# Optimization experiments

Hardware: AMD Instinct MI355X
Metric: run time of the kernel (lower is better)

The kernel has to match this reference:

```python
import jax, jax.numpy as jnp
import numpy as np

D_MODEL = 1024
HEADS = 16
DK = D_MODEL // HEADS  # 64
B, S = 1, 4096


def setup_inputs() -> dict:
    key = jax.random.key(0)
    ks = jax.random.split(key, 11)
    sd = 1.0 / np.sqrt(D_MODEL)
    return {
        "q": jax.random.normal(ks[0], (B, S, D_MODEL), jnp.float32),
        "k": jax.random.normal(ks[1], (B, S, D_MODEL), jnp.float32),
        "v": jax.random.normal(ks[2], (B, S, D_MODEL), jnp.float32),
        "Wq": jax.random.uniform(ks[3], (D_MODEL, D_MODEL), jnp.float32, -sd, sd),
        "bq": jax.random.uniform(ks[4], (D_MODEL,), jnp.float32, -sd, sd),
        "Wk": jax.random.uniform(ks[5], (D_MODEL, DK), jnp.float32, -sd, sd),
        "bk": jax.random.uniform(ks[6], (DK,), jnp.float32, -sd, sd),
        "Wv": jax.random.uniform(ks[7], (D_MODEL, DK), jnp.float32, -sd, sd),
        "bv": jax.random.uniform(ks[8], (DK,), jnp.float32, -sd, sd),
        "Wo": jax.random.uniform(ks[9], (D_MODEL, D_MODEL), jnp.float32, -sd, sd),
        "bo": jax.random.uniform(ks[10], (D_MODEL,), jnp.float32, -sd, sd),
    }


def reference(q, k, v, Wq, bq, Wk, bk, Wv, bv, Wo, bo):
    b, s, d = q.shape
    # projections: q -> [b, H, s, dk]; k, v -> single shared head [b, s, dk]
    qp = (q @ Wq + bq).reshape(b, s, HEADS, DK).transpose(0, 2, 1, 3)
    kp = k @ Wk + bk  # [b, s, dk]
    vp = v @ Wv + bv  # [b, s, dk]
    # NOTE: original module never applies self.scale or dropout — faithful.
    scores = jnp.einsum('bhqd,bkd->bhqk', qp, kp)  # [b, H, s, s]
    attn = jax.nn.softmax(scores, axis=-1)
    out = jnp.einsum('bhqk,bkd->bhqd', attn, vp)  # [b, H, s, dk]
    out = out.transpose(0, 2, 1, 3).reshape(b, s, d)
    return out @ Wo + bo
```

## Files before the change

### kernel.cpp

```cpp
#include <hip/hip_runtime.h>
#include <hip/hip_bf16.h>
#include <stdint.h>

typedef __bf16 bf16_t;
typedef __attribute__((ext_vector_type(8))) __bf16 bf16x8;
typedef __attribute__((ext_vector_type(4))) __bf16 bf16x4;
typedef __attribute__((ext_vector_type(4))) float f32x4;

#define S_LEN 4096
#define DMODEL 1024
#define NHEADS 16
#define DKH 64

#if defined(__has_builtin)
#if __has_builtin(__builtin_amdgcn_exp2f)
#define EXP2F(x) __builtin_amdgcn_exp2f(x)
#endif
#endif
#ifndef EXP2F
#define EXP2F(x) __expf((x)*0.6931471805599453f)
#endif

__device__ __forceinline__ f32x4 mfma16(bf16x8 a, bf16x8 b, f32x4 c) {
  return __builtin_amdgcn_mfma_f32_16x16x32_bf16(a, b, c, 0, 0, 0);
}

template <typename TS>
__device__ __forceinline__ bf16x8 load8_bf16(const TS* g) {
  bf16x8 o;
  if constexpr (sizeof(TS) == 4) {
    const float4 f0 = *(const float4*)(g);
    const float4 f1 = *(const float4*)(g + 4);
    o[0] = (bf16_t)f0.x; o[1] = (bf16_t)f0.y; o[2] = (bf16_t)f0.z; o[3] = (bf16_t)f0.w;
    o[4] = (bf16_t)f1.x; o[5] = (bf16_t)f1.y; o[6] = (bf16_t)f1.z; o[7] = (bf16_t)f1.w;
  } else {
    o = *(const bf16x8*)(g);
  }
  return o;
}

template <typename TS>
__device__ __forceinline__ void stage_tile64(const TS* __restrict__ g, int gstride,
                                             bf16_t* lds, int rows, int tid) {
  for (int i = tid; i < rows * 8; i += 256) {
    const int row = i >> 3, j = i & 7;
    const int c = j ^ (row & 7);
    bf16x8 v = load8_bf16(g + (size_t)row * gstride + j * 8);
    *(bf16x8*)((char*)lds + row * 128 + c * 16) = v;
  }
}

__device__ __forceinline__ bf16x8 frag64(const bf16_t* lds, int row, int g) {
  return *(const bf16x8*)((const char*)lds + row * 128 + ((g ^ (row & 7)) * 16));
}

__device__ __forceinline__ void gload16(const bf16_t* g, bf16_t* lds) {
  __builtin_amdgcn_global_load_lds(
      (const __attribute__((address_space(1))) unsigned int*)g,
      (__attribute__((address_space(3))) unsigned int*)lds, 16, 0, 0);
}

__global__ __launch_bounds__(256) void convert_bf16(const float* __restrict__ src,
                                                    bf16_t* __restrict__ dst) {
  const size_t i = (size_t)(blockIdx.x * 256 + threadIdx.x) * 8;
  bf16x8 v = load8_bf16(src + i);
  *(bf16x8*)(dst + i) = v;
}

__global__ __launch_bounds__(256) void prep_weights(const float* __restrict__ Wq,
                                                    const float* __restrict__ Wo,
                                                    const float* __restrict__ Wk,
                                                    const float* __restrict__ Wv,
                                                    const float* __restrict__ qsrc,
                                                    bf16_t* __restrict__ Wqt,
                                                    bf16_t* __restrict__ Wot,
                                                    bf16_t* __restrict__ Wkt,
                                                    bf16_t* __restrict__ Wvt,
                                                    bf16_t* __restrict__ qdst) {
  const int b = blockIdx.x;
  const int tid = threadIdx.x;
  if (b >= 544) {
    const size_t i = ((size_t)(b - 544) * 256 + tid) * 8;
    bf16x8 v = load8_bf16(qsrc + i);
    *(bf16x8*)(qdst + i) = v;
    return;
  }
  const float* src; bf16_t* dst; int ss, ds_, bx, by;
  if (b < 256)      { src = Wq; dst = Wqt; ss = 1024; ds_ = 1024; bx = b & 15;         by = b >> 4; }
  else if (b < 512) { src = Wo; dst = Wot; ss = 1024; ds_ = 1024; bx = (b - 256) & 15; by = (b - 256) >> 4; }
  else if (b < 528) { src = Wk; dst = Wkt; ss = 64;   ds_ = 1024; bx = 0;              by = b - 512; }
  else              { src = Wv; dst = Wvt; ss = 64;   ds_ = 1024; bx = 0;              by = b - 528; }

  __shared__ bf16_t t[64][65];
  const int r0 = by * 64, c0 = bx * 64;
#pragma unroll
  for (int it = 0; it < 2; ++it) {
    int idx = tid + it * 256;
    int r = idx >> 3, c8 = idx & 7;
    bf16x8 v = load8_bf16(src + (size_t)(r0 + r) * ss + c0 + c8 * 8);
#pragma unroll
    for (int j = 0; j < 8; ++j) t[c8 * 8 + j][r] = v[j];
  }
  __syncthreads();
#pragma unroll
  for (int it = 0; it < 2; ++it) {
    int idx = tid + it * 256;
    int r = idx >> 3, c8 = idx & 7;
    bf16x8 v;
#pragma unroll
    for (int j = 0; j < 8; ++j) v[j] = t[r][c8 * 8 + j];
    *(bf16x8*)(dst + (size_t)(c0 + r) * ds_ + r0 + c8 * 8) = v;
  }
}

template <typename TC>
__global__ __launch_bounds__(256) void gemm_nt_dma(const bf16_t* __restrict__ A, int lda,
                                                   const bf16_t* __restrict__ Bt, int ldb,
                                                   const float* __restrict__ bias,
                                                   TC* __restrict__ C, int ldc, int K,
                                                   float escale) {
  constexpr int BM = 128, BN = 64;
  __shared__ __align__(16) bf16_t As[2][BM * 64];
  __shared__ __align__(16) bf16_t Bs[2][BN * 64];
  const int tid = threadIdx.x, l = tid & 63, w = tid >> 6;
  const int lr = l & 15, quad = l >> 4;
  const int m0 = blockIdx.y * BM, n0 = blockIdx.x * BN;
  const int wm = w * 32;

  const int srow = l >> 3;
  const int sch = (l & 7) ^ srow;
  const bf16_t* a0 = A + (size_t)(m0 + w * 32 + srow) * lda + sch * 8;
  const bf16_t* b0 = Bt + (size_t)(n0 + w * 16 + srow) * ldb + sch * 8;

  f32x4 zero = {0.f, 0.f, 0.f, 0.f};
  f32x4 acc[2][4];
#pragma unroll
  for (int i = 0; i < 2; ++i)
#pragma unroll
    for (int j = 0; j < 4; ++j) acc[i][j] = zero;

  const int nt = K >> 6;

#pragma unroll
  for (int sub = 0; sub < 4; ++sub)
    gload16(a0 + (size_t)sub * 8 * lda, &As[0][(w * 32 + sub * 8) * 64]);
#pragma unroll
  for (int sub = 0; sub < 2; ++sub)
    gload16(b0 + (size_t)sub * 8 * ldb, &Bs[0][(w * 16 + sub * 8) * 64]);
  asm volatile("s_waitcnt vmcnt(0)" ::: "memory");
  __builtin_amdgcn_s_barrier();
  asm volatile("" ::: "memory");

  for (int t = 0; t < nt; ++t) {
    const int cur = t & 1;
    if (t + 1 < nt) {
#pragma unroll
      for (int sub = 0; sub < 4; ++sub)
        gload16(a0 + (size_t)(t + 1) * 64 + (size_t)sub * 8 * lda,
                &As[cur ^ 1][(w * 32 + sub * 8) * 64]);
#pragma unroll
      for (int sub = 0; sub < 2; ++sub)
        gload16(b0 + (size_t)(t + 1) * 64 + (size_t)sub * 8 * ldb,
                &Bs[cur ^ 1][(w * 16 + sub * 8) * 64]);
    }
    const bf16_t* Ac = &As[cur][0];
    const bf16_t* Bc = &Bs[cur][0];
#pragma unroll
    for (int kc = 0; kc < 2; ++kc) {
      bf16x8 af[2], bfr[4];
#pragma unroll
      for (int rt = 0; rt < 2; ++rt) af[rt] = frag64(Ac, wm + rt * 16 + lr, kc * 4 + quad);
#pragma unroll
      for (int ct = 0; ct < 4; ++ct) bfr[ct] = frag64(Bc, ct * 16 + lr, kc * 4 + quad);
#pragma unroll
      for (int rt = 0; rt < 2; ++rt)
#pragma unroll
        for (int ct = 0; ct < 4; ++ct) acc[rt][ct] = mfma16(af[rt], bfr[ct], acc[rt][ct]);
    }
    asm volatile("s_waitcnt vmcnt(0) lgkmcnt(0)" ::: "memory");
    __builtin_amdgcn_s_barrier();
    asm volatile("" ::: "memory");
  }

#pragma unroll
  for (int rt = 0; rt < 2; ++rt)
#pragma unroll
    for (int ct = 0; ct < 4; ++ct) {
      const int n = n0 + ct * 16 + lr;
      const float bv = bias[n];
      const int mb = m0 + wm + rt * 16 + quad * 4;
#pragma unroll
      for (int r = 0; r < 4; ++r)
        C[(size_t)(mb + r) * ldc + n] = (TC)((acc[rt][ct][r] + bv) * escale);
    }
}

template <int KSPLIT>
__global__ __launch_bounds__(256) void gemm_projkv_partial(const float* __restrict__ Ak,
                                                           const float* __restrict__ Av,
                                                           const bf16_t* __restrict__ Wkt,
                                                           const bf16_t* __restrict__ Wvt,
                                                           float* __restrict__ Pk,
                                                           float* __restrict__ Pv) {
  const float* A = blockIdx.z ? Av : Ak;
  const bf16_t* Bt = blockIdx.z ? Wvt : Wkt;
  float* part = blockIdx.z ? Pv : Pk;

  __shared__ __align__(16) bf16_t As[128 * 64];
  __shared__ __align__(16) bf16_t Bs[64 * 64];
  const int tid = threadIdx.x, l = tid & 63, w = tid >> 6;
  const int lr = l & 15, quad = l >> 4;
  const int kp = blockIdx.x, m0 = blockIdx.y * 128;
  const int kBase = kp * (DMODEL / KSPLIT);
  const int wm = w * 32;

  f32x4 zero = {0.f, 0.f, 0.f, 0.f};
  f32x4 acc[2][4];
#pragma unroll
  for (int i = 0; i < 2; ++i)
#pragma unroll
    for (int j = 0; j < 4; ++j) acc[i][j] = zero;

  for (int t = 0; t < (DMODEL / KSPLIT) / 64; ++t) {
    __syncthreads();
    stage_tile64(A + (size_t)m0 * DMODEL + kBase + t * 64, DMODEL, As, 128, tid);
    stage_tile64(Bt + kBase + t * 64, DMODEL, Bs, 64, tid);
    __syncthreads();
#pragma unroll
    for (int kc = 0; kc < 2; ++kc) {
      bf16x8 af[2], bfr[4];
#pragma unroll
      for (int rt = 0; rt < 2; ++rt) af[rt] = frag64(As, wm + rt * 16 + lr, kc * 4 + quad);
#pragma unroll
      for (int ct = 0; ct < 4; ++ct) bfr[ct] = frag64(Bs, ct * 16 + lr, kc * 4 + quad);
#pragma unroll
      for (int rt = 0; rt < 2; ++rt)
#pragma unroll
        for (int ct = 0; ct < 4; ++ct) acc[rt][ct] = mfma16(af[rt], bfr[ct], acc[rt][ct]);
    }
  }
#pragma unroll
  for (int rt = 0; rt < 2; ++rt)
#pragma unroll
    for (int ct = 0; ct < 4; ++ct) {
      const int n = ct * 16 + lr;
      const int mb = m0 + wm + rt * 16 + quad * 4;
#pragma unroll
      for (int r = 0; r < 4; ++r)
        part[(size_t)kp * S_LEN * 64 + (size_t)(mb + r) * 64 + n] = acc[rt][ct][r];
    }
}

__global__ __launch_bounds__(512) void reduce_kv(const float* __restrict__ Pk,
                                                 const float* __restrict__ Pv,
                                                 const float* __restrict__ bk,
                                                 const float* __restrict__ bv,
                                                 bf16_t* __restrict__ kvb,
                                                 bf16_t* __restrict__ vtb) {
  __shared__ bf16_t t[32][65];
  const int tid = threadIdx.x;
  const int s0 = blockIdx.x * 32;
  const int d = tid & 63;
  const int sgrp = tid >> 6;
  const float bkd = bk[d], bvd = bv[d];
#pragma unroll
  for (int i = 0; i < 4; ++i) {
    const int s_local = sgrp * 4 + i;
    const int gid = (s0 + s_local) * 64 + d;
    float sk = bkd, sv = bvd;
#pragma unroll
    for (int p = 0; p < 8; ++p) {
      sk += Pk[(size_t)p * S_LEN * 64 + gid];
      sv += Pv[(size_t)p * S_LEN * 64 + gid];
    }
    kvb[(size_t)(s0 + s_local) * 128 + d] = (bf16_t)sk;
    kvb[(size_t)(s0 + s_local) * 128 + 64 + d] = (bf16_t)sv;
    t[s_local][d] = (bf16_t)sv;
  }
  __syncthreads();
  if (tid < 256) {
    const int dl = tid >> 2;
    const int s8 = tid & 3;
    bf16x8 v;
#pragma unroll
    for (int j = 0; j < 8; ++j) v[j] = t[s8 * 8 + j][dl];
    *(bf16x8*)(vtb + (size_t)dl * S_LEN + s0 + s8 * 8) = v;
  }
}

__global__ __launch_bounds__(512, 4) void mqa_attn(const bf16_t* __restrict__ qp,
                                                   const bf16_t* __restrict__ kvb,
                                                   const bf16_t* __restrict__ vtb,
                                                   bf16_t* __restrict__ outp) {
  __shared__ __align__(16) char smem[49152];
  bf16_t* Ks = (bf16_t*)smem;
  bf16_t* Vs = (bf16_t*)(smem + 16384);
  char*   Ps = smem + 32768;

  const int tid = threadIdx.x, l = tid & 63, w = tid >> 6;
  const int lr = l & 15, quad = l >> 4;
  const int wq = w >> 1, wk = w & 1;
  const int h = blockIdx.y;
  const int q0 = blockIdx.x * 128;
  const int qrA = q0 + wq * 32 + lr;
  const int qrB = qrA + 16;
  char* Pw = Ps + w * 2048;

  const int srow = w * 8 + (l >> 3);
  const int schunk = (l & 7) ^ (srow & 7);
  const bf16_t* ksrc = kvb + (size_t)srow * 128 + schunk * 8;
  const bf16_t* vsrc = vtb + (size_t)srow * S_LEN + schunk * 8;

  const bf16_t* qbA = qp + (size_t)qrA * DMODEL + h * DKH;
  const bf16x8 qfA0 = *(const bf16x8*)(qbA + quad * 8);
  const bf16x8 qfA1 = *(const bf16x8*)(qbA + 32 + quad * 8);
  const bf16_t* qbB = qp + (size_t)qrB * DMODEL + h * DKH;
  const bf16x8 qfB0 = *(const bf16x8*)(qbB + quad * 8);
  const bf16x8 qfB1 = *(const bf16x8*)(qbB + 32 + quad * 8);

  f32x4 zero = {0.f, 0.f, 0.f, 0.f};
  f32x4 o[4][2];
#pragma unroll
  for (int dt = 0; dt < 4; ++dt) { o[dt][0] = zero; o[dt][1] = zero; }
  float liA = 0.f, liB = 0.f;

  gload16(ksrc, Ks + w * 512);
  gload16(vsrc, Vs + w * 512);
  asm volatile("s_waitcnt vmcnt(0)" ::: "memory");
  __builtin_amdgcn_s_barrier();
  asm volatile("" ::: "memory");

  for (int t = 0; t < S_LEN / 64; ++t) {
    const int cur = t & 1;
    if (t + 1 < S_LEN / 64) {
      gload16(ksrc + (size_t)(t + 1) * 8192, Ks + (cur ^ 1) * 4096 + w * 512);
      gload16(vsrc + (size_t)(t + 1) * 64, Vs + (cur ^ 1) * 4096 + w * 512);
    }
    const bf16_t* Kc = Ks + cur * 4096;
    const bf16_t* Vc = Vs + cur * 4096;

    f32x4 st[2][2];
#pragma unroll
    for (int kt = 0; kt < 2; ++kt) {
      const int krow = wk * 32 + kt * 16 + lr;
      const bf16x8 kf0 = frag64(Kc, krow, quad);
      const bf16x8 kf1 = frag64(Kc, krow, 4 + quad);
      f32x4 a0 = mfma16(kf0, qfA0, zero);
      a0 = mfma16(kf1, qfA1, a0);
      st[kt][0] = a0;
      f32x4 a1 = mfma16(kf0, qfB0, zero);
      a1 = mfma16(kf1, qfB1, a1);
      st[kt][1] = a1;
    }

#pragma unroll
    for (int kt = 0; kt < 2; ++kt)
#pragma unroll
      for (int qt = 0; qt < 2; ++qt) {
        bf16x4 pk;
        float rs = 0.f;
#pragma unroll
        for (int r = 0; r < 4; ++r) {
          const float p = EXP2F(st[kt][qt][r]);
          rs += p;
          pk[r] = (bf16_t)p;
        }
        if (qt == 0) liA += rs; else liB += rs;
        *(bf16x4*)(Pw + lr * 128 +
                   ((((qt << 2) + (kt << 1) + (quad >> 1)) ^ (lr & 7)) << 4) +
                   ((quad & 1) << 3)) = pk;
      }
    asm volatile("s_waitcnt lgkmcnt(0)" ::: "memory");

    const bf16x8 pf0 = *(const bf16x8*)(Pw + lr * 128 + ((quad ^ (lr & 7)) << 4));
    const bf16x8 pf1 = *(const bf16x8*)(Pw + lr * 128 + (((4 + quad) ^ (lr & 7)) << 4));
#pragma unroll
    for (int dt = 0; dt < 4; ++dt) {
      const bf16x8 vf = frag64(Vc, dt * 16 + lr, wk * 4 + quad);
      o[dt][0] = mfma16(vf, pf0, o[dt][0]);
      o[dt][1] = mfma16(vf, pf1, o[dt][1]);
    }

    asm volatile("s_waitcnt vmcnt(0) lgkmcnt(0)" ::: "memory");
    __builtin_amdgcn_s_barrier();
    asm volatile("" ::: "memory");
  }

  liA += __shfl_xor(liA, 16, 64);
  liA += __shfl_xor(liA, 32, 64);
  liB += __shfl_xor(liB, 16, 64);
  liB += __shfl_xor(liB, 32, 64);

  float* liBuf = (float*)Ps;
  if (quad == 0) {
    liBuf[w * 32 + lr] = liA;
    liBuf[w * 32 + 16 + lr] = liB;
  }
  float* Obuf = (float*)smem;
  if (wk == 1) {
#pragma unroll
    for (int dt = 0; dt < 4; ++dt)
#pragma unroll
      for (int qt = 0; qt < 2; ++qt)
        *(f32x4*)(&Obuf[wq * 2048 + (qt * 16 + lr) * 64 + dt * 16 + quad * 4]) = o[dt][qt];
  }
  __syncthreads();
  if (wk == 0) {
    const float ltA = liA + liBuf[(w ^ 1) * 32 + lr];
    const float ltB = liB + liBuf[(w ^ 1) * 32 + 16 + lr];
    const float invA = 1.f / ltA;
    const float invB = 1.f / ltB;
#pragma unroll
    for (int dt = 0; dt < 4; ++dt) {
      const f32x4 pA = *(const f32x4*)(&Obuf[wq * 2048 + lr * 64 + dt * 16 + quad * 4]);
      const f32x4 pB = *(const f32x4*)(&Obuf[wq * 2048 + (16 + lr) * 64 + dt * 16 + quad * 4]);
      bf16x4 ovA, ovB;
#pragma unroll
      for (int rg = 0; rg < 4; ++rg) {
        ovA[rg] = (bf16_t)((o[dt][0][rg] + pA[rg]) * invA);
        ovB[rg] = (bf16_t)((o[dt][1][rg] + pB[rg]) * invB);
      }
      *(bf16x4*)(outp + (size_t)qrA * DMODEL + h * DKH + dt * 16 + quad * 4) = ovA;
      *(bf16x4*)(outp + (size_t)qrB * DMODEL + h * DKH + dt * 16 + quad * 4) = ovB;
    }
  }
}

extern "C" void kernel_launch(void* const* d_in, const int* in_sizes, int n_in,
                              void* d_out, int out_size, void* d_ws, size_t ws_size,
                              hipStream_t stream) {
  const float* q  = (const float*)d_in[0];
  const float* k  = (const float*)d_in[1];
  const float* v  = (const float*)d_in[2];
  const float* Wq = (const float*)d_in[3];
  const float* bq = (const float*)d_in[4];
  const float* Wk = (const float*)d_in[5];
  const float* bk = (const float*)d_in[6];
  const float* Wv = (const float*)d_in[7];
  const float* bv = (const float*)d_in[8];
  const float* Wo = (const float*)d_in[9];
  const float* bo = (const float*)d_in[10];
  float* out = (float*)d_out;
  char* ws = (char*)d_ws;

  const size_t MB = 1u << 20;
  bf16_t* Wqt = (bf16_t*)(ws);
  bf16_t* Wot = (bf16_t*)(ws + 2 * MB);
  bf16_t* Wkt = (bf16_t*)(ws + 4 * MB);
  bf16_t* Wvt = (bf16_t*)(ws + 4 * MB + 131072);
  bf16_t* kvb = (bf16_t*)(ws + 4 * MB + 524288);
  bf16_t* vtb = (bf16_t*)(ws + 5 * MB + 524288);
  float*  Pk   = (float*)(ws + 6 * MB);
  float*  Pv   = (float*)(ws + 14 * MB);
  bf16_t* qp   = (bf16_t*)(ws + 14 * MB);
  bf16_t* attn = (bf16_t*)(ws + 6 * MB);

  const bool bigws = ws_size >= (size_t)30 * MB;
  bf16_t* qb = bigws ? (bf16_t*)(ws + 22 * MB) : (bf16_t*)(ws + 6 * MB);

  dim3 B(256);
  prep_weights<<<dim3(bigws ? 2592 : 544), B, 0, stream>>>(Wq, Wo, Wk, Wv, q,
                                                           Wqt, Wot, Wkt, Wvt, qb);

  gemm_projkv_partial<8><<<dim3(8, 32, 2), B, 0, stream>>>(k, v, Wkt, Wvt, Pk, Pv);
  reduce_kv<<<dim3(128), dim3(512), 0, stream>>>(Pk, Pv, bk, bv, kvb, vtb);

  if (!bigws) convert_bf16<<<dim3(2048), B, 0, stream>>>(q, qb);
  gemm_nt_dma<bf16_t><<<dim3(16, 32), B, 0, stream>>>(qb, 1024, Wqt, 1024, bq, qp, 1024, 1024,
                                                      1.44269504088896340736f);

  mqa_attn<<<dim3(32, 16), dim3(512), 0, stream>>>(qp, kvb, vtb, attn);

  gemm_nt_dma<float><<<dim3(16, 32), B, 0, stream>>>(attn, 1024, Wot, 1024, bo, out, 1024, 1024,
                                                     1.0f);
}
```

Baseline: 236.3 us.

## Merge Q projection and split-K KV projection into one launch

On the large-workspace path, the Q projection GEMM and the K/V partial projection GEMMs now run inside a single kernel (mid_gemms), with the block index choosing which body to run. The K/V split-K factor drops from 8 to 4 so both fit in one grid of 768 blocks. The aim is to remove a kernel launch and its tail, and to let the small K/V work fill the GPU alongside the Q GEMM. In exchange, each K/V block does more serial K work, and the shared 48KB LDS footprint may lower occupancy for the projkv blocks.

Measured after the change: 230.3 us, median of 2. 1.03x faster.

```diff
diff --git a/kernel.cpp b/kernel.cpp
--- a/kernel.cpp
+++ b/kernel.cpp
@@ -114,23 +114,110 @@
 }
 
 template <typename TC>
+__device__ __forceinline__ void gemm_body_dma(char* smem,
+                                              const bf16_t* __restrict__ A, int lda,
+                                              const bf16_t* __restrict__ Bt, int ldb,
+                                              const float* __restrict__ bias,
+                                              TC* __restrict__ C, int ldc, int K,
+                                              float escale, int m0, int n0) {
+  constexpr int BM = 128, BN = 64;
+  bf16_t* As = (bf16_t*)smem;
+  bf16_t* Bs = (bf16_t*)(smem + 32768);
+  const int tid = threadIdx.x, l = tid & 63, w = tid >> 6;
+  const int lr = l & 15, quad = l >> 4;
+  const int wm = w * 32;
+
+  const int srow = l >> 3;
+  const int sch = (l & 7) ^ srow;
+  const bf16_t* a0 = A + (size_t)(m0 + w * 32 + srow) * lda + sch * 8;
+  const bf16_t* b0 = Bt + (size_t)(n0 + w * 16 + srow) * ldb + sch * 8;
+
+  f32x4 zero = {0.f, 0.f, 0.f, 0.f};
+  f32x4 acc[2][4];
+#pragma unroll
+  for (int i = 0; i < 2; ++i)
+#pragma unroll
+    for (int j = 0; j < 4; ++j) acc[i][j] = zero;
+
+  const int nt = K >> 6;
+
+#pragma unroll
+  for (int sub = 0; sub < 4; ++sub)
+    gload16(a0 + (size_t)sub * 8 * lda, &As[(w * 32 + sub * 8) * 64]);
+#pragma unroll
+  for (int sub = 0; sub < 2; ++sub)
+    gload16(b0 + (size_t)sub * 8 * ldb, &Bs[(w * 16 + sub * 8) * 64]);
+  asm volatile("s_waitcnt vmcnt(0)" ::: "memory");
+  __builtin_amdgcn_s_barrier();
+  asm volatile("" ::: "memory");
+
+  for (int t = 0; t < nt; ++t) {
+    const int cur = t & 1;
+    if (t + 1 < nt) {
+#pragma unroll
+      for (int sub = 0; sub < 4; ++sub)
+        gload16(a0 + (size_t)(t + 1) * 64 + (size_t)sub * 8 * lda,
+                &As[(cur ^ 1) * BM * 64 + (w * 32 + sub * 8) * 64]);
+#pragma unroll
+      for (int sub = 0; sub < 2; ++sub)
+        gload16(b0 + (size_t)(t + 1) * 64 + (size_t)sub * 8 * ldb,
+                &Bs[(cur ^ 1) * BN * 64 + (w * 16 + sub * 8) * 64]);
+    }
+    const bf16_t* Ac = &As[cur * BM * 64];
+    const bf16_t* Bc = &Bs[cur * BN * 64];
+#pragma unroll
+    for (int kc = 0; kc < 2; ++kc) {
+      bf16x8 af[2], bfr[4];
+#pragma unroll
+      for (int rt = 0; rt < 2; ++rt) af[rt] = frag64(Ac, wm + rt * 16 + lr, kc * 4 + quad);
+#pragma unroll
+      for (int ct = 0; ct < 4; ++ct) bfr[ct] = frag64(Bc, ct * 16 + lr, kc * 4 + quad);
+#pragma unroll
+      for (int rt = 0; rt < 2; ++rt)
+#pragma unroll
+        for (int ct = 0; ct < 4; ++ct) acc[rt][ct] = mfma16(af[rt], bfr[ct], acc[rt][ct]);
+    }
+    asm volatile("s_waitcnt vmcnt(0) lgkmcnt(0)" ::: "memory");
+    __builtin_amdgcn_s_barrier();
+    asm volatile("" ::: "memory");
+  }
+
+#pragma unroll
+  for (int rt = 0; rt < 2; ++rt)
+#pragma unroll
+    for (int ct = 0; ct < 4; ++ct) {
+      const int n = n0 + ct * 16 + lr;
+      const float bv = bias[n];
+      const int mb = m0 + wm + rt * 16 + quad * 4;
+#pragma unroll
+      for (int r = 0; r < 4; ++r)
+        C[(size_t)(mb + r) * ldc + n] = (TC)((acc[rt][ct][r] + bv) * escale);
+    }
+}
+
+template <typename TC>
 __global__ __launch_bounds__(256) void gemm_nt_dma(const bf16_t* __restrict__ A, int lda,
                                                    const bf16_t* __restrict__ Bt, int ldb,
                                                    const float* __restrict__ bias,
                                                    TC* __restrict__ C, int ldc, int K,
                                                    float escale) {
-  constexpr int BM = 128, BN = 64;
-  __shared__ __align__(16) bf16_t As[2][BM * 64];
-  __shared__ __align__(16) bf16_t Bs[2][BN * 64];
+  __shared__ __align__(16) char smem[49152];
+  gemm_body_dma<TC>(smem, A, lda, Bt, ldb, bias, C, ldc, K, escale,
+                    blockIdx.y * 128, blockIdx.x * 64);
+}
+
+template <int KSPLIT>
+__device__ __forceinline__ void projkv_body(char* smem,
+                                            const float* __restrict__ A,
+                                            const bf16_t* __restrict__ Bt,
+                                            float* __restrict__ part,
+                                            int kp, int m0) {
+  bf16_t* As = (bf16_t*)smem;
+  bf16_t* Bs = (bf16_t*)(smem + 16384);
   const int tid = threadIdx.x, l = tid & 63, w = tid >> 6;
   const int lr = l & 15, quad = l >> 4;
-  const int m0 = blockIdx.y * BM, n0 = blockIdx.x * BN;
+  const int kBase = kp * (DMODEL / KSPLIT);
   const int wm = w * 32;
-
-  const int srow = l >> 3;
-  const int sch = (l & 7) ^ srow;
-  const bf16_t* a0 = A + (size_t)(m0 + w * 32 + srow) * lda + sch * 8;
-  const bf16_t* b0 = Bt + (size_t)(n0 + w * 16 + srow) * ldb + sch * 8;
 
   f32x4 zero = {0.f, 0.f, 0.f, 0.f};
   f32x4 acc[2][4];
@@ -139,59 +226,33 @@
 #pragma unroll
     for (int j = 0; j < 4; ++j) acc[i][j] = zero;
 
-  const int nt = K >> 6;
-
-#pragma unroll
-  for (int sub = 0; sub < 4; ++sub)
-    gload16(a0 + (size_t)sub * 8 * lda, &As[0][(w * 32 + sub * 8) * 64]);
-#pragma unroll
-  for (int sub = 0; sub < 2; ++sub)
-    gload16(b0 + (size_t)sub * 8 * ldb, &Bs[0][(w * 16 + sub * 8) * 64]);
-  asm volatile("s_waitcnt vmcnt(0)" ::: "memory");
-  __builtin_amdgcn_s_barrier();
-  asm volatile("" ::: "memory");
-
-  for (int t = 0; t < nt; ++t) {
-    const int cur = t & 1;
-    if (t + 1 < nt) {
-#pragma unroll
-      for (int sub = 0; sub < 4; ++sub)
-        gload16(a0 + (size_t)(t + 1) * 64 + (size_t)sub * 8 * lda,
-                &As[cur ^ 1][(w * 32 + sub * 8) * 64]);
-#pragma unroll
-      for (int sub = 0; sub < 2; ++sub)
-        gload16(b0 + (size_t)(t + 1) * 64 + (size_t)sub * 8 * ldb,
-                &Bs[cur ^ 1][(w * 16 + sub * 8) * 64]);
-    }
-    const bf16_t* Ac = &As[cur][0];
-    const bf16_t* Bc = &Bs[cur][0];
+  for (int t = 0; t < (DMODEL / KSPLIT) / 64; ++t) {
+    __syncthreads();
+    stage_tile64(A + (size_t)m0 * DMODEL + kBase + t * 64, DMODEL, As, 128, tid);
+    stage_tile64(Bt + kBase + t * 64, DMODEL, Bs, 64, tid);
+    __syncthreads();
 #pragma unroll
     for (int kc = 0; kc < 2; ++kc) {
       bf16x8 af[2], bfr[4];
 #pragma unroll
-      for (int rt = 0; rt < 2; ++rt) af[rt] = frag64(Ac, wm + rt * 16 + lr, kc * 4 + quad);
-#pragma unroll
-      for (int ct = 0; ct < 4; ++ct) bfr[ct] = frag64(Bc, ct * 16 + lr, kc * 4 + quad);
+      for (int rt = 0; rt < 2; ++rt) af[rt] = frag64(As, wm + rt * 16 + lr, kc * 4 + quad);
+#pragma unroll
+      for (int ct = 0; ct < 4; ++ct) bfr[ct] = frag64(Bs, ct * 16 + lr, kc * 4 + quad);
 #pragma unroll
       for (int rt = 0; rt < 2; ++rt)
 #pragma unroll
         for (int ct = 0; ct < 4; ++ct) acc[rt][ct] = mfma16(af[rt], bfr[ct], acc[rt][ct]);
     }
-    asm volatile("s_waitcnt vmcnt(0) lgkmcnt(0)" ::: "memory");
-    __builtin_amdgcn_s_barrier();
-    asm volatile("" ::: "memory");
-  }
-
+  }
 #pragma unroll
   for (int rt = 0; rt < 2; ++rt)
 #pragma unroll
     for (int ct = 0; ct < 4; ++ct) {
-      const int n = n0 + ct * 16 + lr;
-      const float bv = bias[n];
+      const int n = ct * 16 + lr;
       const int mb = m0 + wm + rt * 16 + quad * 4;
 #pragma unroll
       for (int r = 0; r < 4; ++r)
-        C[(size_t)(mb + r) * ldc + n] = (TC)((acc[rt][ct][r] + bv) * escale);
+        part[(size_t)kp * S_LEN * 64 + (size_t)(mb + r) * 64 + n] = acc[rt][ct][r];
     }
 }
 
@@ -202,55 +263,36 @@
                                                            const bf16_t* __restrict__ Wvt,
                                                            float* __restrict__ Pk,
                                                            float* __restrict__ Pv) {
-  const float* A = blockIdx.z ? Av : Ak;
-  const bf16_t* Bt = blockIdx.z ? Wvt : Wkt;
-  float* part = blockIdx.z ? Pv : Pk;
-
-  __shared__ __align__(16) bf16_t As[128 * 64];
-  __shared__ __align__(16) bf16_t Bs[64 * 64];
-  const int tid = threadIdx.x, l = tid & 63, w = tid >> 6;
-  const int lr = l & 15, quad = l >> 4;
-  const int kp = blockIdx.x, m0 = blockIdx.y * 128;
-  const int kBase = kp * (DMODEL / KSPLIT);
-  const int wm = w * 32;
-
-  f32x4 zero = {0.f, 0.f, 0.f, 0.f};
-  f32x4 acc[2][4];
-#pragma unroll
-  for (int i = 0; i < 2; ++i)
-#pragma unroll
-    for (int j = 0; j < 4; ++j) acc[i][j] = zero;
-
-  for (int t = 0; t < (DMODEL / KSPLIT) / 64; ++t) {
-    __syncthreads();
-    stage_tile64(A + (size_t)m0 * DMODEL + kBase + t * 64, DMODEL, As, 128, tid);
-    stage_tile64(Bt + kBase + t * 64, DMODEL, Bs, 64, tid);
-    __syncthreads();
-#pragma unroll
-    for (int kc = 0; kc < 2; ++kc) {
-      bf16x8 af[2], bfr[4];
-#pragma unroll
-      for (int rt = 0; rt < 2; ++rt) af[rt] = frag64(As, wm + rt * 16 + lr, kc * 4 + quad);
-#pragma unroll
-      for (int ct = 0; ct < 4; ++ct) bfr[ct] = frag64(Bs, ct * 16 + lr, kc * 4 + quad);
-#pragma unroll
-      for (int rt = 0; rt < 2; ++rt)
-#pragma unroll
-        for (int ct = 0; ct < 4; ++ct) acc[rt][ct] = mfma16(af[rt], bfr[ct], acc[rt][ct]);
-    }
-  }
-#pragma unroll
-  for (int rt = 0; rt < 2; ++rt)
-#pragma unroll
-    for (int ct = 0; ct < 4; ++ct) {
-      const int n = ct * 16 + lr;
-      const int mb = m0 + wm + rt * 16 + quad * 4;
-#pragma unroll
-      for (int r = 0; r < 4; ++r)
-        part[(size_t)kp * S_LEN * 64 + (size_t)(mb + r) * 64 + n] = acc[rt][ct][r];
-    }
-}
-
+  __shared__ __align__(16) char smem[24576];
+  projkv_body<KSPLIT>(smem, blockIdx.z ? Av : Ak, blockIdx.z ? Wvt : Wkt,
+                      blockIdx.z ? Pv : Pk, blockIdx.x, blockIdx.y * 128);
+}
+
+__global__ __launch_bounds__(256) void mid_gemms(const bf16_t* __restrict__ qb,
+                                                 const bf16_t* __restrict__ Wqt,
+                                                 const float* __restrict__ bq,
+                                                 bf16_t* __restrict__ qp,
+                                                 const float* __restrict__ k,
+                                                 const float* __restrict__ v,
+                                                 const bf16_t* __restrict__ Wkt,
+                                                 const bf16_t* __restrict__ Wvt,
+                                                 float* __restrict__ Pk,
+                                                 float* __restrict__ Pv,
+                                                 float escale) {
+  __shared__ __align__(16) char smem[49152];
+  const int flat = blockIdx.x;
+  if (flat < 512) {
+    gemm_body_dma<bf16_t>(smem, qb, 1024, Wqt, 1024, bq, qp, 1024, 1024, escale,
+                          (flat >> 4) * 128, (flat & 15) * 64);
+  } else {
+    const int j = flat - 512;
+    const int z = j >> 7;
+    const int jj = j & 127;
+    projkv_body<4>(smem, z ? v : k, z ? Wvt : Wkt, z ? Pv : Pk, jj & 3, (jj >> 2) * 128);
+  }
+}
+
+template <int KSPLIT>
 __global__ __launch_bounds__(512) void reduce_kv(const float* __restrict__ Pk,
                                                  const float* __restrict__ Pv,
                                                  const float* __restrict__ bk,
@@ -269,7 +311,7 @@
     const int gid = (s0 + s_local) * 64 + d;
     float sk = bkd, sv = bvd;
 #pragma unroll
-    for (int p = 0; p < 8; ++p) {
+    for (int p = 0; p < KSPLIT; ++p) {
       sk += Pk[(size_t)p * S_LEN * 64 + gid];
       sv += Pv[(size_t)p * S_LEN * 64 + gid];
     }
@@ -450,27 +492,39 @@
   bf16_t* Wvt = (bf16_t*)(ws + 4 * MB + 131072);
   bf16_t* kvb = (bf16_t*)(ws + 4 * MB + 524288);
   bf16_t* vtb = (bf16_t*)(ws + 5 * MB + 524288);
-  float*  Pk   = (float*)(ws + 6 * MB);
-  float*  Pv   = (float*)(ws + 14 * MB);
-  bf16_t* qp   = (bf16_t*)(ws + 14 * MB);
-  bf16_t* attn = (bf16_t*)(ws + 6 * MB);
 
   const bool bigws = ws_size >= (size_t)30 * MB;
-  bf16_t* qb = bigws ? (bf16_t*)(ws + 22 * MB) : (bf16_t*)(ws + 6 * MB);
-
   dim3 B(256);
-  prep_weights<<<dim3(bigws ? 2592 : 544), B, 0, stream>>>(Wq, Wo, Wk, Wv, q,
-                                                           Wqt, Wot, Wkt, Wvt, qb);
-
-  gemm_projkv_partial<8><<<dim3(8, 32, 2), B, 0, stream>>>(k, v, Wkt, Wvt, Pk, Pv);
-  reduce_kv<<<dim3(128), dim3(512), 0, stream>>>(Pk, Pv, bk, bv, kvb, vtb);
-
-  if (!bigws) convert_bf16<<<dim3(2048), B, 0, stream>>>(q, qb);
-  gemm_nt_dma<bf16_t><<<dim3(16, 32), B, 0, stream>>>(qb, 1024, Wqt, 1024, bq, qp, 1024, 1024,
-                                                      1.44269504088896340736f);
-
-  mqa_attn<<<dim3(32, 16), dim3(512), 0, stream>>>(qp, kvb, vtb, attn);
-
-  gemm_nt_dma<float><<<dim3(16, 32), B, 0, stream>>>(attn, 1024, Wot, 1024, bo, out, 1024, 1024,
-                                                     1.0f);
-}
+  const float LOG2E = 1.44269504088896340736f;
+
+  if (bigws) {
+    float*  Pk   = (float*)(ws + 6 * MB);
+    float*  Pv   = (float*)(ws + 10 * MB);
+    bf16_t* qp   = (bf16_t*)(ws + 14 * MB);
+    bf16_t* qb   = (bf16_t*)(ws + 22 * MB);
+    bf16_t* attn = (bf16_t*)(ws + 6 * MB);
+
+    prep_weights<<<dim3(2592), B, 0, stream>>>(Wq, Wo, Wk, Wv, q, Wqt, Wot, Wkt, Wvt, qb);
+    mid_gemms<<<dim3(768), B, 0, stream>>>(qb, Wqt, bq, qp, k, v, Wkt, Wvt, Pk, Pv, LOG2E);
+    reduce_kv<4><<<dim3(128), dim3(512), 0, stream>>>(Pk, Pv, bk, bv, kvb, vtb);
+    mqa_attn<<<dim3(32, 16), dim3(512), 0, stream>>>(qp, kvb, vtb, attn);
+    gemm_nt_dma<float><<<dim3(16, 32), B, 0, stream>>>(attn, 1024, Wot, 1024, bo, out,
+                                                       1024, 1024, 1.0f);
+  } else {
+    float*  Pk   = (float*)(ws + 6 * MB);
+    float*  Pv   = (float*)(ws + 14 * MB);
+    bf16_t* qp   = (bf16_t*)(ws + 14 * MB);
+    bf16_t* qb   = (bf16_t*)(ws + 6 * MB);
+    bf16_t* attn = (bf16_t*)(ws + 6 * MB);
+
+    prep_weights<<<dim3(544), B, 0, stream>>>(Wq, Wo, Wk, Wv, q, Wqt, Wot, Wkt, Wvt, qb);
+    gemm_projkv_partial<8><<<dim3(8, 32, 2), B, 0, stream>>>(k, v, Wkt, Wvt, Pk, Pv);
+    reduce_kv<8><<<dim3(128), dim3(512), 0, stream>>>(Pk, Pv, bk, bv, kvb, vtb);
+    convert_bf16<<<dim3(2048), B, 0, stream>>>(q, qb);
+    gemm_nt_dma<bf16_t><<<dim3(16, 32), B, 0, stream>>>(qb, 1024, Wqt, 1024, bq, qp,
+                                                        1024, 1024, LOG2E);
+    mqa_attn<<<dim3(32, 16), dim3(512), 0, stream>>>(qp, kvb, vtb, attn);
+    gemm_nt_dma<float><<<dim3(16, 32), B, 0, stream>>>(attn, 1024, Wot, 1024, bo, out,
+                                                       1024, 1024, 1.0f);
+  }
+}
```
